# Kernel optimization log

Hardware: AMD Instinct MI355X
Metric: run time of the kernel (lower is better)

Reference implementation:

```python
import jax, jax.numpy as jnp
import numpy as np

B, F, NUM_LAYERS, T, DEPTH, C = 256, 128, 4, 2048, 6, 100
L = 2 ** DEPTH  # num_leaves = 64

# bit pattern of the oblivious tree: bit d of leaf_idx (MSB-first),
# matching (leaf_idx // (L >> (d+1))) % 2 in the original double loop
_BITS = np.stack([(np.arange(L) // (L >> (d + 1))) % 2 for d in range(DEPTH)])  # [DEPTH, L]


def setup_inputs() -> dict:
    key = jax.random.key(0)
    k = jax.random.split(key, 5)
    x = jax.random.normal(k[0], (B, F), dtype=jnp.float32)
    sel_W = jax.random.normal(k[1], (NUM_LAYERS, T * DEPTH, F), dtype=jnp.float32) * 0.05
    sel_b = jax.random.normal(k[2], (NUM_LAYERS, T * DEPTH), dtype=jnp.float32) * 0.01
    out_W = jax.random.normal(k[3], (C, NUM_LAYERS * T * L), dtype=jnp.float32) * 0.002
    out_b = jax.random.normal(k[4], (C,), dtype=jnp.float32) * 0.01
    return {"x": x, "sel_W": sel_W, "sel_b": sel_b, "out_W": out_W, "out_b": out_b}


def reference(x, sel_W, sel_b, out_W, out_b):
    bits = jnp.asarray(_BITS, dtype=x.dtype)  # [DEPTH, L]
    layer_outputs = []
    for i in range(NUM_LAYERS):
        # feature selector linear -> [B, T, DEPTH] threshold responses
        fv = jax.nn.sigmoid(x @ sel_W[i].T + sel_b[i]).reshape(B, T, DEPTH)
        # leaf probability = prod over depth of (left or right prob per bit)
        leaf = jnp.ones((B, T, L), dtype=x.dtype)
        for d in range(DEPTH):  # fixed small structural loop (depth=6)
            p = fv[:, :, d:d + 1]                     # [B, T, 1] left prob
            bit = bits[d]                             # [L]
            leaf = leaf * (p * (1.0 - bit) + (1.0 - p) * bit)
        layer_outputs.append(leaf.reshape(B, T * L))
    combined = jnp.concatenate(layer_outputs, axis=1)  # [B, NUM_LAYERS*T*L]
    return combined @ out_W.T + out_b
```

## Files before the change

### kernel.cpp

```cpp
#include <hip/hip_runtime.h>
#include <hip/hip_bf16.h>

#define BB 256
#define FF 128
#define CC 100
#define KG 256
#define ITPB 32
#define NMACRO 16

typedef short bf16x8 __attribute__((ext_vector_type(8)));
typedef float f32x4 __attribute__((ext_vector_type(4)));
typedef _Float16 f16x8 __attribute__((ext_vector_type(8)));

static __device__ inline unsigned short f2bf(float f) {
    unsigned u = __float_as_uint(f);
    u += 0x7fffu + ((u >> 16) & 1u);
    return (unsigned short)(u >> 16);
}
static __device__ inline float bf2f(unsigned short h) {
    return __uint_as_float(((unsigned)h) << 16);
}
static __device__ inline unsigned pk2(float a, float b) {
    __hip_bfloat162 h = __float22bfloat162_rn(float2{a, b});
    union { __hip_bfloat162 h2; unsigned u; } cv; cv.h2 = h;
    return cv.u;
}
static __device__ inline void gl_lds16(const float* g, float* l) {
    __builtin_amdgcn_global_load_lds(
        (const __attribute__((address_space(1))) void*)g,
        (__attribute__((address_space(3))) void*)l, 16, 0, 0);
}

__global__ __launch_bounds__(256) void fv_kernel(
    const float* __restrict__ x, const float* __restrict__ selW,
    const float* __restrict__ selb, unsigned short* __restrict__ fvout)
{
    __shared__ unsigned short wt[128 * 136];
    __shared__ unsigned short xt[128 * 136];
    __shared__ float sb[128];

    const int tid = threadIdx.x;
    const int m0 = blockIdx.x * 128;
    const int n0 = blockIdx.y * 128;

    #pragma unroll 4
    for (int pass = 0; pass < 16; ++pass) {
        int idx = pass * 256 + tid;
        int r = idx >> 5, f4 = idx & 31;
        float4 v = *((const float4*)(selW + (size_t)(m0 + r) * FF) + f4);
        float4 vx = *((const float4*)(x + (size_t)(n0 + r) * FF) + f4);
        ushort4 h;
        h.x = f2bf(v.x); h.y = f2bf(v.y); h.z = f2bf(v.z); h.w = f2bf(v.w);
        *(ushort4*)(wt + r * 136 + f4 * 4) = h;
        ushort4 hx;
        hx.x = f2bf(vx.x); hx.y = f2bf(vx.y); hx.z = f2bf(vx.z); hx.w = f2bf(vx.w);
        *(ushort4*)(xt + r * 136 + f4 * 4) = hx;
    }
    if (tid < 128) sb[tid] = selb[m0 + tid];
    __syncthreads();

    const int w = tid >> 6, lane = tid & 63;
    const int q = lane >> 4, l15 = lane & 15;
    const int mq = w & 1, nq = w >> 1;

    f32x4 zero4 = {0.f, 0.f, 0.f, 0.f};
    f32x4 acc[4][4];
    #pragma unroll
    for (int i = 0; i < 4; ++i)
        #pragma unroll
        for (int j = 0; j < 4; ++j) acc[i][j] = zero4;

    #pragma unroll
    for (int ch = 0; ch < 4; ++ch) {
        bf16x8 a[4];
        #pragma unroll
        for (int ms = 0; ms < 4; ++ms)
            a[ms] = *(const bf16x8*)(wt + (mq * 64 + ms * 16 + l15) * 136 + ch * 32 + q * 8);
        #pragma unroll
        for (int ns = 0; ns < 4; ++ns) {
            bf16x8 bfr = *(const bf16x8*)(xt + (nq * 64 + ns * 16 + l15) * 136 + ch * 32 + q * 8);
            #pragma unroll
            for (int ms = 0; ms < 4; ++ms)
                acc[ms][ns] = __builtin_amdgcn_mfma_f32_16x16x32_bf16(a[ms], bfr, acc[ms][ns], 0, 0, 0);
        }
    }

    #pragma unroll
    for (int ms = 0; ms < 4; ++ms) {
        int rowl = mq * 64 + ms * 16 + q * 4;
        #pragma unroll
        for (int ns = 0; ns < 4; ++ns) {
            int b = n0 + nq * 64 + ns * 16 + l15;
            #pragma unroll
            for (int reg = 0; reg < 4; ++reg) {
                int row = m0 + rowl + reg;
                float z = acc[ms][ns][reg] + sb[rowl + reg];
                float p = 1.0f / (1.0f + __expf(-z));
                fvout[(size_t)row * 256 + b] = f2bf(p);
            }
        }
    }
}

__global__ __launch_bounds__(256, 2) void main_gemm(
    const unsigned short* __restrict__ fv, const float* __restrict__ outW,
    _Float16* __restrict__ part16)
{
    __shared__ float buf[2][8192];

    const int tid = threadIdx.x;
    const int kg = blockIdx.x;
    const int cg = blockIdx.y;
    const int w = tid >> 6, lane = tid & 63;
    const int q = lane >> 4, l15 = lane & 15;
    const int qh = q >> 1, ql = q & 1;
    const int cmax = cg ? 43 : 55;
    const int half = lane >> 5;

    f32x4 zero4 = {0.f, 0.f, 0.f, 0.f};
    f32x4 acc[4][4];
    #pragma unroll
    for (int i = 0; i < 4; ++i)
        #pragma unroll
        for (int j = 0; j < 4; ++j) acc[i][j] = zero4;

    const unsigned short* fvp = fv + tid;
    unsigned short fvh[2][12];

    #define ISSUE_GROUP(mm, nb)                                                  \
    {                                                                            \
        const size_t g0 = (size_t)kg * 2048 + (size_t)(mm) * 128;                \
        _Pragma("unroll")                                                        \
        for (int j = 0; j < 8; ++j) {                                            \
            const int rbase = w * 16 + 2 * j;                                    \
            const int r = rbase + half;                                          \
            const int s = r & 7;                                                 \
            const int slot = ((lane & 31) + s) & 31;                             \
            const int rc = r > cmax ? cmax : r;                                  \
            const int c = cg * 56 + rc;                                          \
            gl_lds16(outW + (size_t)c * 524288 + g0 + slot * 4,                  \
                     &buf[nb][rbase * 128]);                                     \
        }                                                                        \
        const int it0 = kg * ITPB + (mm) * 2;                                    \
        _Pragma("unroll")                                                        \
        for (int e = 0; e < 12; ++e)                                             \
            fvh[nb][e] = fvp[((size_t)(it0 + (e >= 6 ? 1 : 0)) * 6 + (e % 6)) * 256]; \
    }

    ISSUE_GROUP(0, 0);
    ISSUE_GROUP(1, 1);

    #pragma unroll 2
    for (int m = 0; m < NMACRO; ++m) {
        const int cur = m & 1;

        asm volatile("s_waitcnt vmcnt(20)\n\ts_barrier" ::: "memory");

        bf16x8 bfr[4][4];
        #pragma unroll
        for (int ch = 0; ch < 4; ++ch) {
            #pragma unroll
            for (int nt = 0; nt < 4; ++nt) {
                const int r = nt * 16 + l15;
                const int s = r & 7;
                const int sl0 = ((ch * 8 + q * 2) - s) & 31;
                const int sl1 = ((ch * 8 + q * 2 + 1) - s) & 31;
                f32x4 lo = *(const f32x4*)&buf[cur][r * 128 + sl0 * 4];
                f32x4 hi = *(const f32x4*)&buf[cur][r * 128 + sl1 * 4];
                union { bf16x8 v; unsigned u[4]; } bu;
                bu.u[0] = pk2(lo[0], lo[1]);
                bu.u[1] = pk2(lo[2], lo[3]);
                bu.u[2] = pk2(hi[0], hi[1]);
                bu.u[3] = pk2(hi[2], hi[3]);
                bfr[ch][nt] = bu.v;
            }
        }

        #pragma unroll
        for (int itl = 0; itl < 2; ++itl) {
            float p0 = bf2f(fvh[cur][itl * 6 + 0]);
            float p1 = bf2f(fvh[cur][itl * 6 + 1]);
            float p2 = bf2f(fvh[cur][itl * 6 + 2]);
            float p3 = bf2f(fvh[cur][itl * 6 + 3]);
            float p4 = bf2f(fvh[cur][itl * 6 + 4]);
            float p5 = bf2f(fvh[cur][itl * 6 + 5]);

            bf16x8 afr[4][2];
            #pragma unroll
            for (int ms = 0; ms < 4; ++ms) {
                const int src = ms * 16 + l15;
                float s0 = __shfl(p0, src, 64);
                float s1 = __shfl(p1, src, 64);
                float s2 = __shfl(p2, src, 64);
                float s3 = __shfl(p3, src, 64);
                float s4 = __shfl(p4, src, 64);
                float s5 = __shfl(p5, src, 64);
                float t1 = qh ? (1.f - s1) : s1;
                float A0 = s0 * t1;
                float A1 = (1.f - s0) * t1;
                float t2 = ql ? (1.f - s2) : s2;
                float Bv0 = t2 * s3;
                float Bv1 = t2 * (1.f - s3);
                float n4 = 1.f - s4, n5 = 1.f - s5;
                float Cv0 = s4 * s5, Cv1 = s4 * n5, Cv2 = n4 * s5, Cv3 = n4 * n5;
                #pragma unroll
                for (int chl = 0; chl < 2; ++chl) {
                    float A = chl ? A1 : A0;
                    float ab0 = A * Bv0, ab1 = A * Bv1;
                    union { bf16x8 v; unsigned u[4]; } bu;
                    bu.u[0] = pk2(ab0 * Cv0, ab0 * Cv1);
                    bu.u[1] = pk2(ab0 * Cv2, ab0 * Cv3);
                    bu.u[2] = pk2(ab1 * Cv0, ab1 * Cv1);
                    bu.u[3] = pk2(ab1 * Cv2, ab1 * Cv3);
                    afr[ms][chl] = bu.v;
                }
            }
            #pragma unroll
            for (int chl = 0; chl < 2; ++chl) {
                const int ch = itl * 2 + chl;
                #pragma unroll
                for (int nt = 0; nt < 4; ++nt)
                    #pragma unroll
                    for (int ms = 0; ms < 4; ++ms)
                        acc[ms][nt] = __builtin_amdgcn_mfma_f32_16x16x32_bf16(
                            afr[ms][chl], bfr[ch][nt], acc[ms][nt], 0, 0, 0);
            }
        }

        asm volatile("s_waitcnt lgkmcnt(0)\n\ts_barrier" ::: "memory");

        const int mn = (m + 2 < NMACRO) ? (m + 2) : m;
        ISSUE_GROUP(mn, cur);
    }

    const int slotmax = cg ? 44 : 56;
    #pragma unroll
    for (int ms = 0; ms < 4; ++ms) {
        const int brow = w * 64 + ms * 16 + q * 4;
        #pragma unroll
        for (int nt = 0; nt < 4; ++nt) {
            const int slot = nt * 16 + l15;
            if (slot < slotmax) {
                const int c = cg * 56 + slot;
                #pragma unroll
                for (int reg = 0; reg < 4; ++reg)
                    part16[((size_t)(brow + reg) * KG + kg) * 112 + c] =
                        (_Float16)acc[ms][nt][reg];
            }
        }
    }
    #undef ISSUE_GROUP
}

__global__ __launch_bounds__(256) void reduce_k(
    const _Float16* __restrict__ part16, const float* __restrict__ outb,
    float* __restrict__ out)
{
    __shared__ float red[16 * 112];
    const int b = blockIdx.x;
    const int tid = threadIdx.x;
    const f16x8* slice = (const f16x8*)(part16 + (size_t)b * (KG * 112));

    if (tid < 224) {
        const int c8 = tid % 14;
        const int kgs = tid / 14;
        float s[8];
        #pragma unroll
        for (int j = 0; j < 8; ++j) s[j] = 0.f;
        #pragma unroll 4
        for (int i = 0; i < 16; ++i) {
            f16x8 v = slice[i * 224 + tid];
            #pragma unroll
            for (int j = 0; j < 8; ++j) s[j] += (float)v[j];
        }
        #pragma unroll
        for (int j = 0; j < 8; ++j) red[kgs * 112 + c8 * 8 + j] = s[j];
    }
    __syncthreads();
    if (tid < CC) {
        float r = outb[tid];
        #pragma unroll
        for (int k = 0; k < 16; ++k) r += red[k * 112 + tid];
        out[b * CC + tid] = r;
    }
}

extern "C" void kernel_launch(void* const* d_in, const int* in_sizes, int n_in,
                              void* d_out, int out_size, void* d_ws, size_t ws_size,
                              hipStream_t stream) {
    const float* x    = (const float*)d_in[0];
    const float* selW = (const float*)d_in[1];
    const float* selb = (const float*)d_in[2];
    const float* outW = (const float*)d_in[3];
    const float* outb = (const float*)d_in[4];
    float* out = (float*)d_out;

    unsigned short* fv = (unsigned short*)d_ws;
    _Float16* part16 = (_Float16*)((char*)d_ws + 25165824);

    fv_kernel<<<dim3(384, 2), 256, 0, stream>>>(x, selW, selb, fv);
    main_gemm<<<dim3(KG, 2), 256, 0, stream>>>(fv, outW, part16);
    reduce_k<<<BB, 256, 0, stream>>>(part16, outb, out);
}
```

Before: 350.6 us.

## Load outW directly into registers, drop LDS staging, double K-split groups

```diff
diff --git a/kernel.cpp b/kernel.cpp
--- a/kernel.cpp
+++ b/kernel.cpp
@@ -4,9 +4,8 @@
 #define BB 256
 #define FF 128
 #define CC 100
-#define KG 256
-#define ITPB 32
-#define NMACRO 16
+#define KG 512
+#define ITPB 16
 
 typedef short bf16x8 __attribute__((ext_vector_type(8)));
 typedef float f32x4 __attribute__((ext_vector_type(4)));
@@ -24,11 +23,6 @@
     __hip_bfloat162 h = __float22bfloat162_rn(float2{a, b});
     union { __hip_bfloat162 h2; unsigned u; } cv; cv.h2 = h;
     return cv.u;
-}
-static __device__ inline void gl_lds16(const float* g, float* l) {
-    __builtin_amdgcn_global_load_lds(
-        (const __attribute__((address_space(1))) void*)g,
-        (__attribute__((address_space(3))) void*)l, 16, 0, 0);
 }
 
 __global__ __launch_bounds__(256) void fv_kernel(
@@ -106,8 +100,6 @@
     const unsigned short* __restrict__ fv, const float* __restrict__ outW,
     _Float16* __restrict__ part16)
 {
-    __shared__ float buf[2][8192];
-
     const int tid = threadIdx.x;
     const int kg = blockIdx.x;
     const int cg = blockIdx.y;
@@ -115,7 +107,6 @@
     const int q = lane >> 4, l15 = lane & 15;
     const int qh = q >> 1, ql = q & 1;
     const int cmax = cg ? 43 : 55;
-    const int half = lane >> 5;
 
     f32x4 zero4 = {0.f, 0.f, 0.f, 0.f};
     f32x4 acc[4][4];
@@ -124,114 +115,101 @@
         #pragma unroll
         for (int j = 0; j < 4; ++j) acc[i][j] = zero4;
 
+    const float* rowp[4];
+    #pragma unroll
+    for (int nt = 0; nt < 4; ++nt) {
+        int r = nt * 16 + l15;
+        int rc = r > cmax ? cmax : r;
+        rowp[nt] = outW + (size_t)(cg * 56 + rc) * 524288 + q * 8;
+    }
+
     const unsigned short* fvp = fv + tid;
-    unsigned short fvh[2][12];
-
-    #define ISSUE_GROUP(mm, nb)                                                  \
-    {                                                                            \
-        const size_t g0 = (size_t)kg * 2048 + (size_t)(mm) * 128;                \
-        _Pragma("unroll")                                                        \
-        for (int j = 0; j < 8; ++j) {                                            \
-            const int rbase = w * 16 + 2 * j;                                    \
-            const int r = rbase + half;                                          \
-            const int s = r & 7;                                                 \
-            const int slot = ((lane & 31) + s) & 31;                             \
-            const int rc = r > cmax ? cmax : r;                                  \
-            const int c = cg * 56 + rc;                                          \
-            gl_lds16(outW + (size_t)c * 524288 + g0 + slot * 4,                  \
-                     &buf[nb][rbase * 128]);                                     \
-        }                                                                        \
-        const int it0 = kg * ITPB + (mm) * 2;                                    \
-        _Pragma("unroll")                                                        \
-        for (int e = 0; e < 12; ++e)                                             \
-            fvh[nb][e] = fvp[((size_t)(it0 + (e >= 6 ? 1 : 0)) * 6 + (e % 6)) * 256]; \
-    }
-
-    ISSUE_GROUP(0, 0);
-    ISSUE_GROUP(1, 1);
+
+    float4 bbuf[2][16];
+    unsigned short pvb[2][6];
+
+    #define ISSUE(itt, nb)                                                      \
+    {                                                                           \
+        const size_t kbase = (size_t)(itt) * 64;                                \
+        _Pragma("unroll")                                                       \
+        for (int ch = 0; ch < 2; ++ch)                                          \
+            _Pragma("unroll")                                                   \
+            for (int nt = 0; nt < 4; ++nt) {                                    \
+                _Pragma("unroll")                                               \
+                for (int half = 0; half < 2; ++half)                            \
+                    bbuf[nb][ch * 8 + nt * 2 + half] =                          \
+                        *(const float4*)(rowp[nt] + kbase + ch * 32 + half * 4);\
+            }                                                                   \
+        _Pragma("unroll")                                                       \
+        for (int d = 0; d < 6; ++d)                                             \
+            pvb[nb][d] = fvp[((size_t)(itt) * 6 + d) * 256];                    \
+    }
+
+    ISSUE(kg * ITPB, 0);
 
     #pragma unroll 2
-    for (int m = 0; m < NMACRO; ++m) {
-        const int cur = m & 1;
-
-        asm volatile("s_waitcnt vmcnt(20)\n\ts_barrier" ::: "memory");
-
-        bf16x8 bfr[4][4];
-        #pragma unroll
-        for (int ch = 0; ch < 4; ++ch) {
+    for (int itl = 0; itl < ITPB; ++itl) {
+        const int cur = itl & 1;
+
+        const int itn = kg * ITPB + (itl + 1 < ITPB ? itl + 1 : itl);
+        ISSUE(itn, cur ^ 1);
+
+        float p0 = bf2f(pvb[cur][0]), p1 = bf2f(pvb[cur][1]);
+        float p2 = bf2f(pvb[cur][2]), p3 = bf2f(pvb[cur][3]);
+        float p4 = bf2f(pvb[cur][4]), p5 = bf2f(pvb[cur][5]);
+
+        bf16x8 afr[4][2];
+        #pragma unroll
+        for (int ms = 0; ms < 4; ++ms) {
+            const int src = ms * 16 + l15;
+            float s0 = __shfl(p0, src, 64);
+            float s1 = __shfl(p1, src, 64);
+            float s2 = __shfl(p2, src, 64);
+            float s3 = __shfl(p3, src, 64);
+            float s4 = __shfl(p4, src, 64);
+            float s5 = __shfl(p5, src, 64);
+            float t1 = qh ? (1.f - s1) : s1;
+            float A0 = s0 * t1;
+            float A1 = (1.f - s0) * t1;
+            float t2 = ql ? (1.f - s2) : s2;
+            float Bv0 = t2 * s3;
+            float Bv1 = t2 * (1.f - s3);
+            float n4 = 1.f - s4, n5 = 1.f - s5;
+            float Cv0 = s4 * s5, Cv1 = s4 * n5, Cv2 = n4 * s5, Cv3 = n4 * n5;
+            #pragma unroll
+            for (int chl = 0; chl < 2; ++chl) {
+                float A = chl ? A1 : A0;
+                float ab0 = A * Bv0, ab1 = A * Bv1;
+                union { bf16x8 v; unsigned u[4]; } bu;
+                bu.u[0] = pk2(ab0 * Cv0, ab0 * Cv1);
+                bu.u[1] = pk2(ab0 * Cv2, ab0 * Cv3);
+                bu.u[2] = pk2(ab1 * Cv0, ab1 * Cv1);
+                bu.u[3] = pk2(ab1 * Cv2, ab1 * Cv3);
+                afr[ms][chl] = bu.v;
+            }
+        }
+
+        #pragma unroll
+        for (int ch = 0; ch < 2; ++ch) {
             #pragma unroll
             for (int nt = 0; nt < 4; ++nt) {
-                const int r = nt * 16 + l15;
-                const int s = r & 7;
-                const int sl0 = ((ch * 8 + q * 2) - s) & 31;
-                const int sl1 = ((ch * 8 + q * 2 + 1) - s) & 31;
-                f32x4 lo = *(const f32x4*)&buf[cur][r * 128 + sl0 * 4];
-                f32x4 hi = *(const f32x4*)&buf[cur][r * 128 + sl1 * 4];
+                float4 b0 = bbuf[cur][ch * 8 + nt * 2 + 0];
+                float4 b1 = bbuf[cur][ch * 8 + nt * 2 + 1];
                 union { bf16x8 v; unsigned u[4]; } bu;
-                bu.u[0] = pk2(lo[0], lo[1]);
-                bu.u[1] = pk2(lo[2], lo[3]);
-                bu.u[2] = pk2(hi[0], hi[1]);
-                bu.u[3] = pk2(hi[2], hi[3]);
-                bfr[ch][nt] = bu.v;
-            }
-        }
-
-        #pragma unroll
-        for (int itl = 0; itl < 2; ++itl) {
-            float p0 = bf2f(fvh[cur][itl * 6 + 0]);
-            float p1 = bf2f(fvh[cur][itl * 6 + 1]);
-            float p2 = bf2f(fvh[cur][itl * 6 + 2]);
-            float p3 = bf2f(fvh[cur][itl * 6 + 3]);
-            float p4 = bf2f(fvh[cur][itl * 6 + 4]);
-            float p5 = bf2f(fvh[cur][itl * 6 + 5]);
-
-            bf16x8 afr[4][2];
-            #pragma unroll
-            for (int ms = 0; ms < 4; ++ms) {
-                const int src = ms * 16 + l15;
-                float s0 = __shfl(p0, src, 64);
-                float s1 = __shfl(p1, src, 64);
-                float s2 = __shfl(p2, src, 64);
-                float s3 = __shfl(p3, src, 64);
-                float s4 = __shfl(p4, src, 64);
-                float s5 = __shfl(p5, src, 64);
-                float t1 = qh ? (1.f - s1) : s1;
-                float A0 = s0 * t1;
-                float A1 = (1.f - s0) * t1;
-                float t2 = ql ? (1.f - s2) : s2;
-                float Bv0 = t2 * s3;
-                float Bv1 = t2 * (1.f - s3);
-                float n4 = 1.f - s4, n5 = 1.f - s5;
-                float Cv0 = s4 * s5, Cv1 = s4 * n5, Cv2 = n4 * s5, Cv3 = n4 * n5;
+                bu.u[0] = pk2(b0.x, b0.y);
+                bu.u[1] = pk2(b0.z, b0.w);
+                bu.u[2] = pk2(b1.x, b1.y);
+                bu.u[3] = pk2(b1.z, b1.w);
                 #pragma unroll
-                for (int chl = 0; chl < 2; ++chl) {
-                    float A = chl ? A1 : A0;
-                    float ab0 = A * Bv0, ab1 = A * Bv1;
-                    union { bf16x8 v; unsigned u[4]; } bu;
-                    bu.u[0] = pk2(ab0 * Cv0, ab0 * Cv1);
-                    bu.u[1] = pk2(ab0 * Cv2, ab0 * Cv3);
-                    bu.u[2] = pk2(ab1 * Cv0, ab1 * Cv1);
-                    bu.u[3] = pk2(ab1 * Cv2, ab1 * Cv3);
-                    afr[ms][chl] = bu.v;
-                }
-            }
-            #pragma unroll
-            for (int chl = 0; chl < 2; ++chl) {
-                const int ch = itl * 2 + chl;
-                #pragma unroll
-                for (int nt = 0; nt < 4; ++nt)
-                    #pragma unroll
-                    for (int ms = 0; ms < 4; ++ms)
-                        acc[ms][nt] = __builtin_amdgcn_mfma_f32_16x16x32_bf16(
-                            afr[ms][chl], bfr[ch][nt], acc[ms][nt], 0, 0, 0);
-            }
-        }
-
-        asm volatile("s_waitcnt lgkmcnt(0)\n\ts_barrier" ::: "memory");
-
-        const int mn = (m + 2 < NMACRO) ? (m + 2) : m;
-        ISSUE_GROUP(mn, cur);
-    }
+                for (int ms = 0; ms < 4; ++ms)
+                    acc[ms][nt] = __builtin_amdgcn_mfma_f32_16x16x32_bf16(
+                        afr[ms][ch], bu.v, acc[ms][nt], 0, 0, 0);
+            }
+        }
+
+        asm volatile("s_barrier" ::: "memory");
+    }
+    #undef ISSUE
 
     const int slotmax = cg ? 44 : 56;
     #pragma unroll
@@ -249,7 +227,6 @@
             }
         }
     }
-    #undef ISSUE_GROUP
 }
 
 __global__ __launch_bounds__(256) void reduce_k(
@@ -268,7 +245,7 @@
         #pragma unroll
         for (int j = 0; j < 8; ++j) s[j] = 0.f;
         #pragma unroll 4
-        for (int i = 0; i < 16; ++i) {
+        for (int i = 0; i < 32; ++i) {
             f16x8 v = slice[i * 224 + tid];
             #pragma unroll
             for (int j = 0; j < 8; ++j) s[j] += (float)v[j];
```

Result: slower. 442.5 us (+26.2%).
